# Optimization experiments

Measured on AMD Instinct MI355X. Metric: run time of the kernel, lower is better.

Reference implementation:

```python
import jax, jax.numpy as jnp
import numpy as np

N_OBJ, N_REL = 5000, 20000
HID, POOL, N_RELCLS, N_OBJCLS = 512, 4096, 51, 151


def setup_inputs() -> dict:
    key = jax.random.key(0)
    ks = jax.random.split(key, 8)
    s = lambda fi, fo: (2.0 / (fi + fo)) ** 0.5  # xavier-ish scale
    return {
        'edge_ctx': jax.random.normal(ks[0], (N_OBJ, HID), jnp.float32),
        'union_features': jax.random.normal(ks[1], (N_REL, POOL), jnp.float32),
        'W_pe': jax.random.normal(ks[2], (2 * HID, HID), jnp.float32) * (10.0 * (1.0 / HID) ** 0.5),
        'b_pe': jnp.zeros((2 * HID,), jnp.float32),
        'W_pc': jax.random.normal(ks[3], (POOL, 2 * HID), jnp.float32) * s(2 * HID, POOL),
        'b_pc': jnp.zeros((POOL,), jnp.float32),
        'W_cc': jax.random.normal(ks[4], (N_RELCLS, POOL), jnp.float32) * s(POOL, N_RELCLS),
        'b_cc': jnp.zeros((N_RELCLS,), jnp.float32),
        'freq_emb': jax.random.normal(ks[5], (N_OBJCLS * N_OBJCLS, N_RELCLS), jnp.float32) * 0.1,
        'obj_preds': jax.random.randint(ks[6], (N_OBJ,), 0, N_OBJCLS, jnp.int64 if jax.config.jax_enable_x64 else jnp.int32),
        'pair_idx': jax.random.randint(ks[7], (N_REL, 2), 0, N_OBJ, jnp.int64 if jax.config.jax_enable_x64 else jnp.int32),
    }


def reference(edge_ctx, union_features, W_pe, b_pe, W_pc, b_pc, W_cc, b_cc,
              freq_emb, obj_preds, pair_idx):
    # post_emb -> relu -> split into head/tail halves ([N,2,HID] view)
    edge_rep = jax.nn.relu(edge_ctx @ W_pe.T + b_pe)          # [N, 2*HID]
    head_rep, tail_rep = edge_rep[:, :HID], edge_rep[:, HID:]

    hi, ti = pair_idx[:, 0], pair_idx[:, 1]
    prod = jnp.concatenate([head_rep[hi], tail_rep[ti]], axis=-1)  # [R, 2*HID]
    prod_rep = prod @ W_pc.T + b_pc                               # [R, POOL]

    ctx_dists = (prod_rep * union_features) @ W_cc.T + b_cc      # [R, 51]

    # frequency bias: embedding lookup at head_cls * num_obj_cls + tail_cls
    pair_lbl = obj_preds[hi] * N_OBJCLS + obj_preds[ti]
    frq_dists = freq_emb[pair_lbl]                               # [R, 51]
    # dropout p=0.3 is identity in eval mode
    return ctx_dists + frq_dists
```

## Files before the change

### kernel.cpp

```cpp
#include <hip/hip_runtime.h>

typedef unsigned short u16;
typedef unsigned int u32;
typedef __attribute__((ext_vector_type(4))) float f32x4;
typedef __attribute__((ext_vector_type(8))) __bf16 bf16x8;
typedef __attribute__((ext_vector_type(8))) u16 u16x8;

__device__ __forceinline__ u16 f2bf(float x) {
  u32 u = __float_as_uint(x);
  u32 r = (u + 0x7FFFu + ((u >> 16) & 1u)) >> 16;
  return (u16)r;
}

__device__ __forceinline__ float bf2f(u16 b) {
  return __uint_as_float((u32)b << 16);
}

__device__ __forceinline__ void gl16(const void* g, void* l) {
  auto* gp = (__attribute__((address_space(1))) u32*)(g);
  auto* lp = (__attribute__((address_space(3))) u32*)(l);
  __builtin_amdgcn_global_load_lds(gp, lp, 16, 0, 0);
}

__device__ __forceinline__ f32x4 mfma16(bf16x8 a, bf16x8 b, f32x4 c) {
  return __builtin_amdgcn_mfma_f32_16x16x32_bf16(a, b, c, 0, 0, 0);
}


__global__ void k_cvt(const float* __restrict__ in, u16* __restrict__ out, int n8) {
  int i = blockIdx.x * 256 + threadIdx.x;
  if (i >= n8) return;
  const float4* p = (const float4*)in + (long)i * 2;
  float4 a = p[0], b = p[1];
  u16x8 v;
  v[0] = f2bf(a.x); v[1] = f2bf(a.y); v[2] = f2bf(a.z); v[3] = f2bf(a.w);
  v[4] = f2bf(b.x); v[5] = f2bf(b.y); v[6] = f2bf(b.z); v[7] = f2bf(b.w);
  *(u16x8*)(out + (long)i * 8) = v;
}

__global__ void k_cvt_wcc(const float* __restrict__ wcc, u16* __restrict__ out, int n8) {
  int i = blockIdx.x * 256 + threadIdx.x;
  if (i >= n8) return;
  long base = (long)i * 8;
  int row = (int)(base >> 12);
  int col = (int)(base & 4095);
  u16x8 v;
  if (row < 51) {
    const float4* p = (const float4*)(wcc + (long)row * 4096 + col);
    float4 a = p[0], b = p[1];
    v[0] = f2bf(a.x); v[1] = f2bf(a.y); v[2] = f2bf(a.z); v[3] = f2bf(a.w);
    v[4] = f2bf(b.x); v[5] = f2bf(b.y); v[6] = f2bf(b.z); v[7] = f2bf(b.w);
  } else {
#pragma unroll
    for (int j = 0; j < 8; ++j) v[j] = 0;
  }
  *(u16x8*)(out + base) = v;
}

__device__ __forceinline__ void cstep(const char* sA, const char* sB,
                                      const int (&aOff)[4], const int (&bOff)[4],
                                      f32x4 (&acc)[4][4]) {
  bf16x8 af[4], bv[4];
#pragma unroll
  for (int mi = 0; mi < 4; ++mi) af[mi] = *(const bf16x8*)(sA + aOff[mi]);
#pragma unroll
  for (int ni = 0; ni < 4; ++ni) bv[ni] = *(const bf16x8*)(sB + bOff[ni]);
  __builtin_amdgcn_s_setprio(1);
#pragma unroll
  for (int mi = 0; mi < 4; ++mi)
#pragma unroll
    for (int ni = 0; ni < 4; ++ni)
      acc[mi][ni] = mfma16(af[mi], bv[ni], acc[mi][ni]);
  __builtin_amdgcn_s_setprio(0);
}

__global__ __launch_bounds__(256, 2) void k_gemm1(const u16* __restrict__ A, const u16* __restrict__ B,
                                                  const float* __restrict__ bias, u16* __restrict__ outp) {
  __shared__ char lds[65536];
  int bx = blockIdx.x;
  int rb = bx >> 3, nb = bx & 7;
  int rowBase = rb * 128, nBase = nb * 128;
  int t = threadIdx.x, lane = t & 63, wid = t >> 6;
  int wr = wid >> 1, wc = wid & 1, lm = lane & 15, lg = lane >> 4;
  int ar0 = t >> 2, ar1 = 64 + ar0, c4 = t & 3;
  int sw0 = (c4 * 16) ^ (((ar0 >> 1) & 3) << 4);
  int sw1 = (c4 * 16) ^ (((ar1 >> 1) & 3) << 4);
  const char* aS0 = (const char*)(A + (long)min(rowBase + ar0, 4999) * 512) + sw0;
  const char* aS1 = (const char*)(A + (long)min(rowBase + ar1, 4999) * 512) + sw1;
  const char* bS0 = (const char*)(B + (long)(nBase + ar0) * 512) + sw0;
  const char* bS1 = (const char*)(B + (long)(nBase + ar1) * 512) + sw1;
  int t16 = t * 16;
  int aOff[4], bOff[4];
#pragma unroll
  for (int mi = 0; mi < 4; ++mi) { int r = wr * 64 + mi * 16 + lm; aOff[mi] = r * 64 + ((lg * 16) ^ (((r >> 1) & 3) << 4)); }
#pragma unroll
  for (int ni = 0; ni < 4; ++ni) { int r = wc * 64 + ni * 16 + lm; bOff[ni] = r * 64 + ((lg * 16) ^ (((r >> 1) & 3) << 4)); }
  f32x4 acc[4][4] = {};

#define STAGE_G(k, sb) do { \
    gl16(aS0 + (k) * 2, (sb) + t16); gl16(aS1 + (k) * 2, (sb) + 4096 + t16); \
    gl16(bS0 + (k) * 2, (sb) + 8192 + t16); gl16(bS1 + (k) * 2, (sb) + 12288 + t16); \
  } while (0)

  STAGE_G(0, lds);
  STAGE_G(32, lds + 16384);
  STAGE_G(64, lds + 32768);

  int cur = 0, stg = 3;
  for (int kt = 0; kt < 16; ++kt) {
    if (kt < 13) {
      char* sb = lds + stg * 16384;
      STAGE_G((kt + 3) * 32, sb);
    }
    if (kt < 13)       asm volatile("s_waitcnt vmcnt(12)" ::: "memory");
    else if (kt == 13) asm volatile("s_waitcnt vmcnt(8)" ::: "memory");
    else if (kt == 14) asm volatile("s_waitcnt vmcnt(4)" ::: "memory");
    else               asm volatile("s_waitcnt vmcnt(0)" ::: "memory");
    __builtin_amdgcn_s_barrier();
    char* cb = lds + cur * 16384;
    cstep(cb, cb + 8192, aOff, bOff, acc);
    __builtin_amdgcn_s_barrier();
    cur = (cur == 3) ? 0 : cur + 1;
    stg = (stg == 3) ? 0 : stg + 1;
  }
#undef STAGE_G

#pragma unroll
  for (int mi = 0; mi < 4; ++mi)
#pragma unroll
    for (int ni = 0; ni < 4; ++ni) {
      int n = nBase + wc * 64 + ni * 16 + lm;
      float bvv = bias[n];
#pragma unroll
      for (int rg = 0; rg < 4; ++rg) {
        int r = rowBase + wr * 64 + mi * 16 + lg * 4 + rg;
        if (r < 5000) {
          float v = acc[mi][ni][rg] + bvv;
          v = v > 0.f ? v : 0.f;
          outp[(long)r * 1024 + n] = f2bf(v);
        }
      }
    }
}

__global__ __launch_bounds__(256, 2) void k_gemm2(const u16* __restrict__ erep, const u16* __restrict__ wpc,
                                                  const float* __restrict__ bpc, u16* __restrict__ Hout,
                                                  u16* __restrict__ Tout) {
  __shared__ char lds[65536];
  int bx = blockIdx.x;
  int h = (bx >= 1280) ? 1 : 0;
  int rr = bx - h * 1280;
  int rb = rr >> 5, nb = rr & 31;
  int rowBase = rb * 128, nBase = nb * 128;
  u16* outp = h ? Tout : Hout;
  int t = threadIdx.x, lane = t & 63, wid = t >> 6;
  int wr = wid >> 1, wc = wid & 1, lm = lane & 15, lg = lane >> 4;
  int ar0 = t >> 2, ar1 = 64 + ar0, c4 = t & 3;
  int sw0 = (c4 * 16) ^ (((ar0 >> 1) & 3) << 4);
  int sw1 = (c4 * 16) ^ (((ar1 >> 1) & 3) << 4);
  const char* aS0 = (const char*)(erep + (long)min(rowBase + ar0, 4999) * 1024 + h * 512) + sw0;
  const char* aS1 = (const char*)(erep + (long)min(rowBase + ar1, 4999) * 1024 + h * 512) + sw1;
  const char* bS0 = (const char*)(wpc + (long)(nBase + ar0) * 1024 + h * 512) + sw0;
  const char* bS1 = (const char*)(wpc + (long)(nBase + ar1) * 1024 + h * 512) + sw1;
  int t16 = t * 16;
  int aOff[4], bOff[4];
#pragma unroll
  for (int mi = 0; mi < 4; ++mi) { int r = wr * 64 + mi * 16 + lm; aOff[mi] = r * 64 + ((lg * 16) ^ (((r >> 1) & 3) << 4)); }
#pragma unroll
  for (int ni = 0; ni < 4; ++ni) { int r = wc * 64 + ni * 16 + lm; bOff[ni] = r * 64 + ((lg * 16) ^ (((r >> 1) & 3) << 4)); }
  f32x4 acc[4][4] = {};

#define STAGE_G2(k, sb) do { \
    gl16(aS0 + (k) * 2, (sb) + t16); gl16(aS1 + (k) * 2, (sb) + 4096 + t16); \
    gl16(bS0 + (k) * 2, (sb) + 8192 + t16); gl16(bS1 + (k) * 2, (sb) + 12288 + t16); \
  } while (0)

  STAGE_G2(0, lds);
  STAGE_G2(32, lds + 16384);
  STAGE_G2(64, lds + 32768);

  int cur = 0, stg = 3;
  for (int kt = 0; kt < 16; ++kt) {
    if (kt < 13) {
      char* sb = lds + stg * 16384;
      STAGE_G2((kt + 3) * 32, sb);
    }
    if (kt < 13)       asm volatile("s_waitcnt vmcnt(12)" ::: "memory");
    else if (kt == 13) asm volatile("s_waitcnt vmcnt(8)" ::: "memory");
    else if (kt == 14) asm volatile("s_waitcnt vmcnt(4)" ::: "memory");
    else               asm volatile("s_waitcnt vmcnt(0)" ::: "memory");
    __builtin_amdgcn_s_barrier();
    char* cb = lds + cur * 16384;
    cstep(cb, cb + 8192, aOff, bOff, acc);
    __builtin_amdgcn_s_barrier();
    cur = (cur == 3) ? 0 : cur + 1;
    stg = (stg == 3) ? 0 : stg + 1;
  }
#undef STAGE_G2

#pragma unroll
  for (int mi = 0; mi < 4; ++mi)
#pragma unroll
    for (int ni = 0; ni < 4; ++ni) {
      int n = nBase + wc * 64 + ni * 16 + lm;
      float bvv = h ? 0.f : bpc[n];
#pragma unroll
      for (int rg = 0; rg < 4; ++rg) {
        int r = rowBase + wr * 64 + mi * 16 + lg * 4 + rg;
        if (r < 5000) {
          float v = acc[mi][ni][rg] + bvv;
          outp[(long)r * 4096 + n] = f2bf(v);
        }
      }
    }
}

__global__ __launch_bounds__(256, 2) void k_final(
    const u16* __restrict__ H, const u16* __restrict__ T,
    const u16* __restrict__ wcc,
    const float* __restrict__ un,
    const float* __restrict__ bcc, const float* __restrict__ freq,
    const int* __restrict__ preds, const int* __restrict__ pidx,
    float* __restrict__ outp) {
  __shared__ char sU[32768];
  __shared__ int sLbl[128];
  int bx = blockIdx.x;
  int rb = bx >> 2, ps = bx & 3;
  int rowBase = rb * 128;
  int t = threadIdx.x, lane = t & 63, wid = t >> 6;
  int lm = lane & 15, lg = lane >> 4;
  int r16 = t >> 4, c16 = t & 15;

  if (t < 128) {
    int rG = min(rowBase + t, 19999);
    sLbl[t] = preds[pidx[2 * rG]] * 151 + preds[pidx[2 * rG + 1]];
  }

  const u16* hp[8];
  const u16* tp[8];
#pragma unroll
  for (int p = 0; p < 8; ++p) {
    int rG = min(rowBase + p * 16 + r16, 19999);
    hp[p] = H + (long)pidx[2 * rG] * 4096;
    tp[p] = T + (long)pidx[2 * rG + 1] * 4096;
  }

  f32x4 outAcc[2][4] = {};

  for (int chk = 0; chk < 8; ++chk) {
    int pcBase = ps * 1024 + chk * 128;
    if (chk) __builtin_amdgcn_s_barrier();
#pragma unroll
    for (int p = 0; p < 8; ++p) {
      int r = p * 16 + r16;
      long rG = min(rowBase + r, 19999);
      u16x8 h8 = *(const u16x8*)(hp[p] + pcBase + c16 * 8);
      u16x8 t8 = *(const u16x8*)(tp[p] + pcBase + c16 * 8);
      float4 u0 = *(const float4*)(un + rG * 4096 + pcBase + c16 * 8);
      float4 u1 = *(const float4*)(un + rG * 4096 + pcBase + c16 * 8 + 4);
      float uu[8];
      *(float4*)(uu) = u0;
      *(float4*)(uu + 4) = u1;
      u16x8 pv;
#pragma unroll
      for (int j = 0; j < 8; ++j)
        pv[j] = f2bf((bf2f(h8[j]) + bf2f(t8[j])) * uu[j]);
      *(u16x8*)(sU + r * 256 + ((c16 * 16) ^ ((r & 7) << 4))) = pv;
    }
    __syncthreads();

#pragma unroll
    for (int kb = 0; kb < 4; ++kb) {
      bf16x8 aU[2], bW[4];
#pragma unroll
      for (int m2 = 0; m2 < 2; ++m2) {
        int r = wid * 32 + m2 * 16 + lm;
        aU[m2] = *(const bf16x8*)(sU + r * 256 + ((kb * 64 + lg * 16) ^ ((r & 7) << 4)));
      }
#pragma unroll
      for (int ni = 0; ni < 4; ++ni)
        bW[ni] = *(const bf16x8*)(wcc + (long)(ni * 16 + lm) * 4096 + pcBase + kb * 32 + lg * 8);
      __builtin_amdgcn_s_setprio(1);
#pragma unroll
      for (int m2 = 0; m2 < 2; ++m2)
#pragma unroll
        for (int ni = 0; ni < 4; ++ni)
          outAcc[m2][ni] = mfma16(aU[m2], bW[ni], outAcc[m2][ni]);
      __builtin_amdgcn_s_setprio(0);
    }
  }

#pragma unroll
  for (int m2 = 0; m2 < 2; ++m2)
#pragma unroll
    for (int rg = 0; rg < 4; ++rg) {
      int r = wid * 32 + m2 * 16 + lg * 4 + rg;
      int rG = rowBase + r;
      if (rG < 20000) {
#pragma unroll
        for (int ni = 0; ni < 4; ++ni) {
          int c = ni * 16 + lm;
          if (c < 51) {
            float v = outAcc[m2][ni][rg];
            if (ps == 0) v += bcc[c] + freq[(long)sLbl[r] * 51 + c];
            atomicAdd(&outp[(long)rG * 51 + c], v);
          }
        }
      }
    }
}

extern "C" void kernel_launch(void* const* d_in, const int* in_sizes, int n_in,
                              void* d_out, int out_size, void* d_ws, size_t ws_size,
                              hipStream_t stream) {
  const float* edge_ctx = (const float*)d_in[0];
  const float* unionf   = (const float*)d_in[1];
  const float* W_pe     = (const float*)d_in[2];
  const float* b_pe     = (const float*)d_in[3];
  const float* W_pc     = (const float*)d_in[4];
  const float* b_pc     = (const float*)d_in[5];
  const float* W_cc     = (const float*)d_in[6];
  const float* b_cc     = (const float*)d_in[7];
  const float* freq     = (const float*)d_in[8];
  const int*   preds    = (const int*)d_in[9];
  const int*   pidx     = (const int*)d_in[10];
  float* out = (float*)d_out;
  char* ws = (char*)d_ws;

  u16* Hb   = (u16*)(ws + 0);
  u16* Tb   = (u16*)(ws + 40960000);
  u16* erep = (u16*)(ws + 81920000);
  u16* wpcb = (u16*)(ws + 92160000);
  u16* wccb = (u16*)(ws + 100548608);
  u16* ecb  = (u16*)(ws + 101072896);
  u16* wpeb = (u16*)(ws + 106192896);

  hipMemsetAsync(d_out, 0, (size_t)out_size * 4, stream);
  k_cvt<<<1250, 256, 0, stream>>>(edge_ctx, ecb, 320000);
  k_cvt<<<256, 256, 0, stream>>>(W_pe, wpeb, 65536);
  k_cvt<<<2048, 256, 0, stream>>>(W_pc, wpcb, 524288);
  k_cvt_wcc<<<128, 256, 0, stream>>>(W_cc, wccb, 32768);
  k_gemm1<<<320, 256, 0, stream>>>(ecb, wpeb, b_pe, erep);
  k_gemm2<<<2560, 256, 0, stream>>>(erep, wpcb, b_pc, Hb, Tb);
  k_final<<<628, 256, 0, stream>>>(Hb, Tb, wccb, unionf, b_cc, freq, preds, pidx, out);
}
```

Measured before the change: 260.0 us.

## Fuse conversion kernels, widen gemm2 K-tile, prefetch H/T gathers in final kernel

Merges the four fp32-to-bf16 conversion launches into one prep kernel to cut launch overhead. Restructures gemm2 to use 64-wide K tiles with double buffering and an 8-way XOR swizzle, replacing the 4-stage 32-wide pipeline. In the final kernel, H/T gathered rows are register-prefetched one chunk ahead, offsets become 32-bit, and launch bounds are relaxed. These changes raise register pressure and may lower occupancy.

```diff
diff --git a/kernel.cpp b/kernel.cpp
--- a/kernel.cpp
+++ b/kernel.cpp
@@ -26,35 +26,41 @@
   return __builtin_amdgcn_mfma_f32_16x16x32_bf16(a, b, c, 0, 0, 0);
 }
 
-
-__global__ void k_cvt(const float* __restrict__ in, u16* __restrict__ out, int n8) {
-  int i = blockIdx.x * 256 + threadIdx.x;
-  if (i >= n8) return;
-  const float4* p = (const float4*)in + (long)i * 2;
-  float4 a = p[0], b = p[1];
+__device__ __forceinline__ u16x8 cvt8(const float* p) {
+  float4 a = *(const float4*)p, b = *(const float4*)(p + 4);
   u16x8 v;
   v[0] = f2bf(a.x); v[1] = f2bf(a.y); v[2] = f2bf(a.z); v[3] = f2bf(a.w);
   v[4] = f2bf(b.x); v[5] = f2bf(b.y); v[6] = f2bf(b.z); v[7] = f2bf(b.w);
-  *(u16x8*)(out + (long)i * 8) = v;
-}
-
-__global__ void k_cvt_wcc(const float* __restrict__ wcc, u16* __restrict__ out, int n8) {
+  return v;
+}
+
+__global__ void k_prep(const float* __restrict__ ec, const float* __restrict__ wpe,
+                       const float* __restrict__ wpc, const float* __restrict__ wcc,
+                       u16* __restrict__ ecb, u16* __restrict__ wpeb,
+                       u16* __restrict__ wpcb, u16* __restrict__ wccb) {
   int i = blockIdx.x * 256 + threadIdx.x;
-  if (i >= n8) return;
-  long base = (long)i * 8;
-  int row = (int)(base >> 12);
-  int col = (int)(base & 4095);
-  u16x8 v;
-  if (row < 51) {
-    const float4* p = (const float4*)(wcc + (long)row * 4096 + col);
-    float4 a = p[0], b = p[1];
-    v[0] = f2bf(a.x); v[1] = f2bf(a.y); v[2] = f2bf(a.z); v[3] = f2bf(a.w);
-    v[4] = f2bf(b.x); v[5] = f2bf(b.y); v[6] = f2bf(b.z); v[7] = f2bf(b.w);
-  } else {
-#pragma unroll
-    for (int j = 0; j < 8; ++j) v[j] = 0;
-  }
-  *(u16x8*)(out + base) = v;
+  if (i < 320000) {
+    *(u16x8*)(ecb + (long)i * 8) = cvt8(ec + (long)i * 8);
+  } else if (i < 385536) {
+    int j = i - 320000;
+    *(u16x8*)(wpeb + (long)j * 8) = cvt8(wpe + (long)j * 8);
+  } else if (i < 909824) {
+    int j = i - 385536;
+    *(u16x8*)(wpcb + (long)j * 8) = cvt8(wpc + (long)j * 8);
+  } else if (i < 942592) {
+    int j = i - 909824;
+    long base = (long)j * 8;
+    int row = (int)(base >> 12);
+    int col = (int)(base & 4095);
+    u16x8 v;
+    if (row < 51) {
+      v = cvt8(wcc + (long)row * 4096 + col);
+    } else {
+#pragma unroll
+      for (int k = 0; k < 8; ++k) v[k] = 0;
+    }
+    *(u16x8*)(wccb + base) = v;
+  }
 }
 
 __device__ __forceinline__ void cstep(const char* sA, const char* sB,
@@ -71,6 +77,29 @@
 #pragma unroll
     for (int ni = 0; ni < 4; ++ni)
       acc[mi][ni] = mfma16(af[mi], bv[ni], acc[mi][ni]);
+  __builtin_amdgcn_s_setprio(0);
+}
+
+__device__ __forceinline__ void cstep64(const char* buf,
+                                        const int (&aOff)[4][2], const int (&bOff)[4][2],
+                                        f32x4 (&acc)[4][4]) {
+  bf16x8 af[4][2], bv[4][2];
+#pragma unroll
+  for (int mi = 0; mi < 4; ++mi)
+#pragma unroll
+    for (int ks = 0; ks < 2; ++ks) af[mi][ks] = *(const bf16x8*)(buf + aOff[mi][ks]);
+#pragma unroll
+  for (int ni = 0; ni < 4; ++ni)
+#pragma unroll
+    for (int ks = 0; ks < 2; ++ks) bv[ni][ks] = *(const bf16x8*)(buf + bOff[ni][ks]);
+  __builtin_amdgcn_s_setprio(1);
+#pragma unroll
+  for (int ks = 0; ks < 2; ++ks)
+#pragma unroll
+    for (int mi = 0; mi < 4; ++mi)
+#pragma unroll
+      for (int ni = 0; ni < 4; ++ni)
+        acc[mi][ni] = mfma16(af[mi][ks], bv[ni][ks], acc[mi][ni]);
   __builtin_amdgcn_s_setprio(0);
 }
 
@@ -155,48 +184,53 @@
   u16* outp = h ? Tout : Hout;
   int t = threadIdx.x, lane = t & 63, wid = t >> 6;
   int wr = wid >> 1, wc = wid & 1, lm = lane & 15, lg = lane >> 4;
-  int ar0 = t >> 2, ar1 = 64 + ar0, c4 = t & 3;
-  int sw0 = (c4 * 16) ^ (((ar0 >> 1) & 3) << 4);
-  int sw1 = (c4 * 16) ^ (((ar1 >> 1) & 3) << 4);
-  const char* aS0 = (const char*)(erep + (long)min(rowBase + ar0, 4999) * 1024 + h * 512) + sw0;
-  const char* aS1 = (const char*)(erep + (long)min(rowBase + ar1, 4999) * 1024 + h * 512) + sw1;
-  const char* bS0 = (const char*)(wpc + (long)(nBase + ar0) * 1024 + h * 512) + sw0;
-  const char* bS1 = (const char*)(wpc + (long)(nBase + ar1) * 1024 + h * 512) + sw1;
+  int ar = t >> 3, c8 = t & 7;
+  int srcswz = ((c8 ^ (ar & 7)) << 4);
+  const char* aP[4];
+  const char* bP[4];
+#pragma unroll
+  for (int i = 0; i < 4; ++i) {
+    int Ra = min(rowBase + i * 32 + ar, 4999);
+    aP[i] = (const char*)(erep + (long)Ra * 1024 + h * 512) + srcswz;
+    int Rb = nBase + i * 32 + ar;
+    bP[i] = (const char*)(wpc + (long)Rb * 1024 + h * 512) + srcswz;
+  }
   int t16 = t * 16;
-  int aOff[4], bOff[4];
-#pragma unroll
-  for (int mi = 0; mi < 4; ++mi) { int r = wr * 64 + mi * 16 + lm; aOff[mi] = r * 64 + ((lg * 16) ^ (((r >> 1) & 3) << 4)); }
-#pragma unroll
-  for (int ni = 0; ni < 4; ++ni) { int r = wc * 64 + ni * 16 + lm; bOff[ni] = r * 64 + ((lg * 16) ^ (((r >> 1) & 3) << 4)); }
+  int aOff[4][2], bOff[4][2];
+#pragma unroll
+  for (int mi = 0; mi < 4; ++mi)
+#pragma unroll
+    for (int ks = 0; ks < 2; ++ks) {
+      int r = wr * 64 + mi * 16 + lm;
+      aOff[mi][ks] = r * 128 + (((ks * 4 + lg) ^ (r & 7)) << 4);
+    }
+#pragma unroll
+  for (int ni = 0; ni < 4; ++ni)
+#pragma unroll
+    for (int ks = 0; ks < 2; ++ks) {
+      int r = wc * 64 + ni * 16 + lm;
+      bOff[ni][ks] = 16384 + r * 128 + (((ks * 4 + lg) ^ (r & 7)) << 4);
+    }
   f32x4 acc[4][4] = {};
 
-#define STAGE_G2(k, sb) do { \
-    gl16(aS0 + (k) * 2, (sb) + t16); gl16(aS1 + (k) * 2, (sb) + 4096 + t16); \
-    gl16(bS0 + (k) * 2, (sb) + 8192 + t16); gl16(bS1 + (k) * 2, (sb) + 12288 + t16); \
+#define STAGE2(kk, buf) do { \
+    _Pragma("unroll") \
+    for (int i = 0; i < 4; ++i) { \
+      gl16(aP[i] + (kk) * 2, (buf) + i * 4096 + t16); \
+      gl16(bP[i] + (kk) * 2, (buf) + 16384 + i * 4096 + t16); \
+    } \
   } while (0)
 
-  STAGE_G2(0, lds);
-  STAGE_G2(32, lds + 16384);
-  STAGE_G2(64, lds + 32768);
-
-  int cur = 0, stg = 3;
-  for (int kt = 0; kt < 16; ++kt) {
-    if (kt < 13) {
-      char* sb = lds + stg * 16384;
-      STAGE_G2((kt + 3) * 32, sb);
-    }
-    if (kt < 13)       asm volatile("s_waitcnt vmcnt(12)" ::: "memory");
-    else if (kt == 13) asm volatile("s_waitcnt vmcnt(8)" ::: "memory");
-    else if (kt == 14) asm volatile("s_waitcnt vmcnt(4)" ::: "memory");
-    else               asm volatile("s_waitcnt vmcnt(0)" ::: "memory");
-    __builtin_amdgcn_s_barrier();
-    char* cb = lds + cur * 16384;
-    cstep(cb, cb + 8192, aOff, bOff, acc);
-    __builtin_amdgcn_s_barrier();
-    cur = (cur == 3) ? 0 : cur + 1;
-    stg = (stg == 3) ? 0 : stg + 1;
-  }
-#undef STAGE_G2
+  STAGE2(0, lds);
+  for (int kt = 0; kt < 8; ++kt) {
+    if (kt < 7) STAGE2((kt + 1) * 64, lds + (((kt + 1) & 1) ? 32768 : 0));
+    if (kt < 7) asm volatile("s_waitcnt vmcnt(8)" ::: "memory");
+    else        asm volatile("s_waitcnt vmcnt(0)" ::: "memory");
+    __builtin_amdgcn_s_barrier();
+    cstep64(lds + ((kt & 1) ? 32768 : 0), aOff, bOff, acc);
+    __builtin_amdgcn_s_barrier();
+  }
+#undef STAGE2
 
 #pragma unroll
   for (int mi = 0; mi < 4; ++mi)
@@ -215,7 +249,7 @@
     }
 }
 
-__global__ __launch_bounds__(256, 2) void k_final(
+__global__ __launch_bounds__(256) void k_final(
     const u16* __restrict__ H, const u16* __restrict__ T,
     const u16* __restrict__ wcc,
     const float* __restrict__ un,
@@ -236,38 +270,50 @@
     sLbl[t] = preds[pidx[2 * rG]] * 151 + preds[pidx[2 * rG + 1]];
   }
 
-  const u16* hp[8];
-  const u16* tp[8];
+  u32 hoff[8], toff[8], uoff[8];
 #pragma unroll
   for (int p = 0; p < 8; ++p) {
     int rG = min(rowBase + p * 16 + r16, 19999);
-    hp[p] = H + (long)pidx[2 * rG] * 4096;
-    tp[p] = T + (long)pidx[2 * rG + 1] * 4096;
+    hoff[p] = (u32)pidx[2 * rG] * 8192u + (u32)c16 * 16u;
+    toff[p] = (u32)pidx[2 * rG + 1] * 8192u + (u32)c16 * 16u;
+    uoff[p] = (u32)rG * 16384u + (u32)c16 * 32u;
+  }
+  const char* Hc = (const char*)H;
+  const char* Tc = (const char*)T;
+  const char* Uc = (const char*)un;
+  int pc0 = ps * 1024;
+
+  u16x8 ph[8], pt[8];
+#pragma unroll
+  for (int p = 0; p < 8; ++p) {
+    ph[p] = *(const u16x8*)(Hc + hoff[p] + pc0 * 2);
+    pt[p] = *(const u16x8*)(Tc + toff[p] + pc0 * 2);
   }
 
   f32x4 outAcc[2][4] = {};
 
   for (int chk = 0; chk < 8; ++chk) {
-    int pcBase = ps * 1024 + chk * 128;
-    if (chk) __builtin_amdgcn_s_barrier();
+    int pcBase = pc0 + chk * 128;
 #pragma unroll
     for (int p = 0; p < 8; ++p) {
       int r = p * 16 + r16;
-      long rG = min(rowBase + r, 19999);
-      u16x8 h8 = *(const u16x8*)(hp[p] + pcBase + c16 * 8);
-      u16x8 t8 = *(const u16x8*)(tp[p] + pcBase + c16 * 8);
-      float4 u0 = *(const float4*)(un + rG * 4096 + pcBase + c16 * 8);
-      float4 u1 = *(const float4*)(un + rG * 4096 + pcBase + c16 * 8 + 4);
+      float4 u0 = *(const float4*)(Uc + uoff[p] + (u32)pcBase * 4u);
+      float4 u1 = *(const float4*)(Uc + uoff[p] + (u32)pcBase * 4u + 16u);
       float uu[8];
       *(float4*)(uu) = u0;
       *(float4*)(uu + 4) = u1;
       u16x8 pv;
 #pragma unroll
       for (int j = 0; j < 8; ++j)
-        pv[j] = f2bf((bf2f(h8[j]) + bf2f(t8[j])) * uu[j]);
+        pv[j] = f2bf((bf2f(ph[p][j]) + bf2f(pt[p][j])) * uu[j]);
       *(u16x8*)(sU + r * 256 + ((c16 * 16) ^ ((r & 7) << 4))) = pv;
-    }
-    __syncthreads();
+      if (chk < 7) {
+        ph[p] = *(const u16x8*)(Hc + hoff[p] + (u32)(pcBase + 128) * 2u);
+        pt[p] = *(const u16x8*)(Tc + toff[p] + (u32)(pcBase + 128) * 2u);
+      }
+    }
+    asm volatile("s_waitcnt lgkmcnt(0)" ::: "memory");
+    __builtin_amdgcn_s_barrier();
 
 #pragma unroll
     for (int kb = 0; kb < 4; ++kb) {
@@ -288,6 +334,8 @@
           outAcc[m2][ni] = mfma16(aU[m2], bW[ni], outAcc[m2][ni]);
       __builtin_amdgcn_s_setprio(0);
     }
+    asm volatile("s_waitcnt lgkmcnt(0)" ::: "memory");
+    __builtin_amdgcn_s_barrier();
   }
 
 #pragma unroll
@@ -336,10 +384,7 @@
   u16* wpeb = (u16*)(ws + 106192896);
 
   hipMemsetAsync(d_out, 0, (size_t)out_size * 4, stream);
-  k_cvt<<<1250, 256, 0, stream>>>(edge_ctx, ecb, 320000);
-  k_cvt<<<256, 256, 0, stream>>>(W_pe, wpeb, 65536);
-  k_cvt<<<2048, 256, 0, stream>>>(W_pc, wpcb, 524288);
-  k_cvt_wcc<<<128, 256, 0, stream>>>(W_cc, wccb, 32768);
+  k_prep<<<3682, 256, 0, stream>>>(edge_ctx, W_pe, W_pc, W_cc, ecb, wpeb, wpcb, wccb);
   k_gemm1<<<320, 256, 0, stream>>>(ecb, wpeb, b_pe, erep);
   k_gemm2<<<2560, 256, 0, stream>>>(erep, wpcb, b_pc, Hb, Tb);
   k_final<<<628, 256, 0, stream>>>(Hb, Tb, wccb, unionf, b_cc, freq, preds, pidx, out);
```

Result: slower. 305.3 us (+17.4%).
